# Performance work log

Hardware: AMD Instinct MI355X
Metric: run time of the kernel (lower is better)

## Reference

```python
import jax, jax.numpy as jnp
import numpy as np

# tag2index constants
PAD, START, END, T = 0, 14, 15, 16
B, L, V, E, H = 128, 512, 30000, 256, 256


def _lstm(xs, w_ih, w_hh, b, reverse=False):
    """xs: [L, B, E] -> hs: [L, B, H]. PyTorch gate order i,f,g,o."""
    Bsz = xs.shape[1]
    Hd = w_hh.shape[1]
    def cell(carry, xt):
        h, c = carry
        g = xt @ w_ih.T + h @ w_hh.T + b  # [B, 4H]
        i, f, gg, o = jnp.split(g, 4, axis=-1)
        c = jax.nn.sigmoid(f) * c + jax.nn.sigmoid(i) * jnp.tanh(gg)
        h = jax.nn.sigmoid(o) * jnp.tanh(c)
        return (h, c), h
    init = (jnp.zeros((Bsz, Hd), xs.dtype), jnp.zeros((Bsz, Hd), xs.dtype))
    _, hs = jax.lax.scan(cell, init, xs, reverse=reverse)
    return hs


def setup_inputs() -> dict:
    key = jax.random.key(0)
    ks = jax.random.split(key, 12)
    batch_data = jax.random.randint(ks[0], (B, L), 0, V, dtype=jnp.int32)
    # variable-length tags with contiguous trailing PAD (as the model assumes)
    lengths = jax.random.randint(ks[1], (B,), L // 4, L + 1)
    raw_tags = jax.random.randint(ks[2], (B, L), 1, 14, dtype=jnp.int32)  # real tags in [1,14)
    pos = jnp.arange(L)[None, :]
    batch_tag = jnp.where(pos < lengths[:, None], raw_tags, PAD).astype(jnp.int32)
    s = 0.05
    emb = jax.random.normal(ks[3], (V, E), jnp.float32) * s
    w_ih_f = jax.random.normal(ks[4], (4 * H, E), jnp.float32) * s
    w_hh_f = jax.random.normal(ks[5], (4 * H, H), jnp.float32) * s
    b_f = jnp.zeros((4 * H,), jnp.float32)
    w_ih_b = jax.random.normal(ks[6], (4 * H, E), jnp.float32) * s
    w_hh_b = jax.random.normal(ks[7], (4 * H, H), jnp.float32) * s
    b_b = jnp.zeros((4 * H,), jnp.float32)
    w_cls = jax.random.normal(ks[8], (T, 2 * H), jnp.float32) * s
    b_cls = jnp.zeros((T,), jnp.float32)
    transition = jnp.full((T, T), 1.0 / T, jnp.float32)
    return {"batch_data": batch_data, "batch_tag": batch_tag, "emb": emb,
            "w_ih_f": w_ih_f, "w_hh_f": w_hh_f, "b_f": b_f,
            "w_ih_b": w_ih_b, "w_hh_b": w_hh_b, "b_b": b_b,
            "w_cls": w_cls, "b_cls": b_cls, "transition": transition}


def reference(batch_data, batch_tag, emb, w_ih_f, w_hh_f, b_f,
              w_ih_b, w_hh_b, b_b, w_cls, b_cls, transition):
    # ---- BiLSTM encoder ----
    x = emb[batch_data]                      # [B, L, E]
    xs = jnp.moveaxis(x, 1, 0)               # [L, B, E]
    hf = _lstm(xs, w_ih_f, w_hh_f, b_f, reverse=False)
    hb = _lstm(xs, w_ih_b, w_hh_b, b_b, reverse=True)
    out = jnp.moveaxis(jnp.concatenate([hf, hb], axis=-1), 0, 1)  # [B, L, 2H]
    emission = out @ w_cls.T + b_cls          # [B, L, T]
    crf_scores = emission[:, :, None, :] + transition[None, None]  # [B, L, T, T]

    # ---- CRF loss (linear-chain forward algorithm) ----
    mask = batch_tag != PAD                   # [B, L]
    lengths = mask.sum(axis=1)                # [B]
    prev = jnp.concatenate(
        [jnp.full((B, 1), START, batch_tag.dtype), batch_tag[:, :-1]], axis=1)
    idx = (batch_tag + prev * T).astype(jnp.int32)  # flat (prev_tag, cur_tag) index
    flat = crf_scores.reshape(B, L, T * T)
    g = jnp.take_along_axis(flat, idx[:, :, None], axis=2)[..., 0]
    golden_scores = jnp.sum(jnp.where(mask, g, 0.0))

    sc_t = jnp.moveaxis(crf_scores, 1, 0)     # [L, B, T, T]
    init = sc_t[0, :, START, :]               # [B, T] (all lengths >= 1)
    def step(prev_scores, x_t):
        sc, t = x_t
        new = jax.nn.logsumexp(sc + prev_scores[:, :, None], axis=1)  # [B, T]
        active = (lengths > t)[:, None]
        return jnp.where(active, new, prev_scores), None
    final, _ = jax.lax.scan(step, init, (sc_t[1:], jnp.arange(1, L)))
    all_path_scores = jnp.sum(final[:, END])
    loss = (all_path_scores - golden_scores) / B
    return loss
```

## Files before the change

### kernel.cpp

```cpp
#include <hip/hip_runtime.h>

#define Bsz 128
#define Lseq 512
#define Hdim 256
#define Tn 16
#define START_TAG 14
#define END_TAG 15

typedef float f32x4 __attribute__((ext_vector_type(4)));
typedef short s16x8 __attribute__((ext_vector_type(8)));

__device__ __forceinline__ unsigned short f2bf(float f) {
    unsigned int u = __builtin_bit_cast(unsigned int, f);
    u += 0x7fffu + ((u >> 16) & 1u);
    return (unsigned short)(u >> 16);
}
__device__ __forceinline__ float bf2f(unsigned int bits16) {
    return __builtin_bit_cast(float, bits16 << 16);
}
__device__ __forceinline__ float sigmoidf_(float x) {
    return 1.0f / (1.0f + __expf(-x));
}

__global__ void embprep_kernel(const float* __restrict__ emb,
                               unsigned int* __restrict__ embb, int n2) {
    int i = blockIdx.x * blockDim.x + threadIdx.x;
    int stride = gridDim.x * blockDim.x;
    for (; i < n2; i += stride)
        embb[i] = (unsigned int)f2bf(emb[2 * i]) | ((unsigned int)f2bf(emb[2 * i + 1]) << 16);
}

__global__ void wprep_kernel(const float* __restrict__ wih_f, const float* __restrict__ whh_f,
                             const float* __restrict__ wih_b, const float* __restrict__ whh_b,
                             unsigned int* __restrict__ wtile) {
    int bid = blockIdx.x;
    int ki  = bid & 15;
    int tl  = (bid >> 4) & 3;
    int ug  = (bid >> 6) & 15;
    int dir = bid >> 10;
    int t = threadIdx.x;
    int lane = t >> 2, j = t & 3;
    int n = lane & 15, kq = lane >> 4;
    int k0 = ki * 32 + kq * 8 + 2 * j;
    int col = tl * 256 + ug * 16 + n;
    const float* wih = dir ? wih_b : wih_f;
    const float* whh = dir ? whh_b : whh_f;
    float f0, f1;
    if (k0 < 256) { f0 = wih[col * 256 + k0];       f1 = wih[col * 256 + k0 + 1]; }
    else          { f0 = whh[col * 256 + k0 - 256]; f1 = whh[col * 256 + k0 - 255]; }
    wtile[(size_t)bid * 256 + t] = (unsigned int)f2bf(f0) | ((unsigned int)f2bf(f1) << 16);
}

__global__ void lengths_kernel(const int* __restrict__ tag, int* __restrict__ lengths) {
    int b = blockIdx.x;
    int tid = threadIdx.x;
    int cnt = 0;
    for (int l = tid; l < Lseq; l += blockDim.x)
        cnt += (tag[b * Lseq + l] != 0) ? 1 : 0;
    for (int off = 32; off > 0; off >>= 1) cnt += __shfl_down(cnt, off);
    __shared__ int red[4];
    if ((tid & 63) == 0) red[tid >> 6] = cnt;
    __syncthreads();
    if (tid == 0) lengths[b] = red[0] + red[1] + red[2] + red[3];
}

__global__ __launch_bounds__(256, 1) void bilstm_persist(
    const int* __restrict__ bd,
    const unsigned int* __restrict__ embb,
    const unsigned int* __restrict__ wtile,
    const float* __restrict__ b_f, const float* __restrict__ b_b,
    const float* __restrict__ w_cls,
    float* __restrict__ em_f, float* __restrict__ em_b,
    unsigned int* __restrict__ ring,
    int* __restrict__ flags)
{
    const int wg  = blockIdx.x;
    const int dir = wg >> 7;
    const int bg  = (wg >> 4) & 7;
    const int ug  = wg & 15;
    const int grp = dir * 8 + bg;
    const int tid = threadIdx.x;
    const int gb0 = bg * 16;

    __shared__ unsigned int w_lds[16384];
    __shared__ unsigned int h_lds[16 * 132];
    __shared__ float g_lds[4][16][17];
    __shared__ float part_lds[16][17];
    __shared__ float bias_lds[64];
    __shared__ float wcls_lds[256];

    {
        const unsigned int* wsrc = wtile + ((size_t)(dir * 16 + ug) << 14);
        for (int i = 0; i < 16; ++i) {
            int idx = tid + 256 * i;
            uint4 v = *(const uint4*)(wsrc + (size_t)idx * 4);
            *(uint4*)&w_lds[idx * 4] = v;
        }
        if (tid < 64) {
            const float* bias = dir ? b_b : b_f;
            bias_lds[tid] = bias[(tid >> 4) * 256 + ug * 16 + (tid & 15)];
        }
        wcls_lds[tid] = w_cls[(size_t)ug * (2 * Hdim) + dir * Hdim + tid];
    }

    const int wv = tid >> 6;
    const int l  = tid & 63;
    const int n  = l & 15;
    const int kq = l >> 4;
    const int cb = tid >> 4, cu = tid & 15;
    const int em_m = tid >> 4, em_seg = tid & 15;
    float c_reg = 0.f;
    float* emout = dir ? em_b : em_f;
    const int* bd_row = bd + (size_t)(gb0 + n) * Lseq;

    unsigned int* rbase = ring + (size_t)dir * 2 * 16384;

    __syncthreads();

    f32x4 acc_x = {0.f, 0.f, 0.f, 0.f};
    {
        const int t0 = dir ? (Lseq - 1) : 0;
        int tok = bd_row[t0];
        const unsigned int* xsrc = embb + (size_t)tok * 128 + kq * 4;
        #pragma unroll
        for (int ki = 0; ki < 8; ++ki) {
            uint4 xv = *(const uint4*)(xsrc + ki * 16);
            s16x8 a = __builtin_bit_cast(s16x8, xv);
            s16x8 b = *(const s16x8*)&w_lds[((wv * 16 + ki) * 64 + l) * 4];
            acc_x = __builtin_amdgcn_mfma_f32_16x16x32_bf16(a, b, acc_x, 0, 0, 0);
        }
    }

    for (int s = 0; s < Lseq; ++s) {
        const int t = dir ? (Lseq - 1 - s) : s;
        const unsigned int* hprev = rbase + ((s & 1) ^ 1) * 16384;
        unsigned int*       hcur  = rbase + (s & 1) * 16384;

        {
            int m = tid >> 4, q0 = (tid & 15) * 8;
            const unsigned int* src = hprev + (gb0 + m) * 128 + q0;
            unsigned int v[8];
            #pragma unroll
            for (int j = 0; j < 8; ++j)
                v[j] = __hip_atomic_load(src + j, __ATOMIC_RELAXED, __HIP_MEMORY_SCOPE_AGENT);
            *(uint4*)&h_lds[m * 132 + q0]     = make_uint4(v[0], v[1], v[2], v[3]);
            *(uint4*)&h_lds[m * 132 + q0 + 4] = make_uint4(v[4], v[5], v[6], v[7]);
        }
        __syncthreads();

        if (s > 0) {
            const unsigned int* hr = &h_lds[em_m * 132 + em_seg * 8];
            const float* wc = &wcls_lds[em_seg * 16];
            float p = 0.f;
            #pragma unroll
            for (int j = 0; j < 8; ++j) {
                unsigned int v = hr[j];
                p += bf2f(v & 0xffffu) * wc[2 * j] + bf2f(v >> 16) * wc[2 * j + 1];
            }
            part_lds[em_m][em_seg] = p;
        }
        {
            f32x4 acc = acc_x;
            #pragma unroll
            for (int kih = 0; kih < 8; ++kih) {
                s16x8 a = *(const s16x8*)&h_lds[n * 132 + kih * 16 + kq * 4];
                s16x8 b = *(const s16x8*)&w_lds[(((wv * 16) + 8 + kih) * 64 + l) * 4];
                acc = __builtin_amdgcn_mfma_f32_16x16x32_bf16(a, b, acc, 0, 0, 0);
            }
            #pragma unroll
            for (int r = 0; r < 4; ++r)
                g_lds[wv][kq * 4 + r][n] = acc[r];
        }
        __syncthreads();

        {
            float gi = g_lds[0][cb][cu] + bias_lds[cu];
            float gf = g_lds[1][cb][cu] + bias_lds[16 + cu];
            float gg = g_lds[2][cb][cu] + bias_lds[32 + cu];
            float go = g_lds[3][cb][cu] + bias_lds[48 + cu];
            float cn = sigmoidf_(gf) * c_reg + sigmoidf_(gi) * tanhf(gg);
            c_reg = cn;
            float hn = sigmoidf_(go) * tanhf(cn);
            unsigned int hbits = (unsigned int)f2bf(hn);
            unsigned int other = (unsigned int)__shfl_down((int)hbits, 1);
            if ((cu & 1) == 0) {
                unsigned int pk = hbits | (other << 16);
                __hip_atomic_store(hcur + (gb0 + cb) * 128 + ug * 8 + (cu >> 1), pk,
                                   __ATOMIC_RELAXED, __HIP_MEMORY_SCOPE_AGENT);
            }
        }
        if (s > 0 && tid < 16) {
            float ssum = 0.f;
            #pragma unroll
            for (int q = 0; q < 16; ++q) ssum += part_lds[tid][q];
            int t_prev = dir ? (Lseq - s) : (s - 1);
            emout[((size_t)(gb0 + tid) * Lseq + t_prev) * Tn + ug] = ssum;
        }
        __syncthreads();

        if (tid == 0)
            __hip_atomic_store(&flags[((size_t)s * 16 + grp) * 16 + ug], 1,
                               __ATOMIC_RELAXED, __HIP_MEMORY_SCOPE_AGENT);

        if (s + 1 < Lseq) {
            const int tn = dir ? (Lseq - 2 - s) : (s + 1);
            int tok = bd_row[tn];
            const unsigned int* xsrc = embb + (size_t)tok * 128 + kq * 4;
            f32x4 ax = {0.f, 0.f, 0.f, 0.f};
            #pragma unroll
            for (int ki = 0; ki < 8; ++ki) {
                uint4 xv = *(const uint4*)(xsrc + ki * 16);
                s16x8 a = __builtin_bit_cast(s16x8, xv);
                s16x8 b = *(const s16x8*)&w_lds[((wv * 16 + ki) * 64 + l) * 4];
                ax = __builtin_amdgcn_mfma_f32_16x16x32_bf16(a, b, ax, 0, 0, 0);
            }
            acc_x = ax;
        }

        if (wv == 0) {
            const int* flg = &flags[((size_t)s * 16 + grp) * 16];
            while (true) {
                int v = (l < 16)
                    ? __hip_atomic_load(&flg[l], __ATOMIC_RELAXED, __HIP_MEMORY_SCOPE_AGENT)
                    : 1;
                if (__all(v != 0)) break;
                __builtin_amdgcn_s_sleep(1);
            }
        }
        __syncthreads();
    }

    {
        const unsigned int* hlast = rbase + ((Lseq - 1) & 1) * 16384;
        int m = tid >> 4, q0 = (tid & 15) * 8;
        const unsigned int* src = hlast + (gb0 + m) * 128 + q0;
        unsigned int v[8];
        #pragma unroll
        for (int j = 0; j < 8; ++j)
            v[j] = __hip_atomic_load(src + j, __ATOMIC_RELAXED, __HIP_MEMORY_SCOPE_AGENT);
        *(uint4*)&h_lds[m * 132 + q0]     = make_uint4(v[0], v[1], v[2], v[3]);
        *(uint4*)&h_lds[m * 132 + q0 + 4] = make_uint4(v[4], v[5], v[6], v[7]);
        __syncthreads();
        {
            const unsigned int* hr = &h_lds[em_m * 132 + em_seg * 8];
            const float* wc = &wcls_lds[em_seg * 16];
            float p = 0.f;
            #pragma unroll
            for (int j = 0; j < 8; ++j) {
                unsigned int vv = hr[j];
                p += bf2f(vv & 0xffffu) * wc[2 * j] + bf2f(vv >> 16) * wc[2 * j + 1];
            }
            part_lds[em_m][em_seg] = p;
        }
        __syncthreads();
        if (tid < 16) {
            float ssum = 0.f;
            #pragma unroll
            for (int q = 0; q < 16; ++q) ssum += part_lds[tid][q];
            int t_tail = dir ? 0 : (Lseq - 1);
            emout[((size_t)(gb0 + tid) * Lseq + t_tail) * Tn + ug] = ssum;
        }
    }
}

__global__ void golden_kernel(const int* __restrict__ tag,
                              const float* __restrict__ em_f,
                              const float* __restrict__ em_b,
                              const float* __restrict__ b_cls,
                              const float* __restrict__ trans,
                              float* __restrict__ golden)
{
    int b = blockIdx.x;
    int tid = threadIdx.x;
    float s = 0.f;
    for (int l = tid; l < Lseq; l += blockDim.x) {
        int tg = tag[b * Lseq + l];
        if (tg != 0) {
            int prev = (l == 0) ? START_TAG : tag[b * Lseq + l - 1];
            size_t e = ((size_t)b * Lseq + l) * Tn + tg;
            s += em_f[e] + em_b[e] + b_cls[tg] + trans[prev * Tn + tg];
        }
    }
    for (int off = 32; off > 0; off >>= 1) s += __shfl_down(s, off);
    __shared__ float red[4];
    if ((tid & 63) == 0) red[tid >> 6] = s;
    __syncthreads();
    if (tid == 0) atomicAdd(golden, red[0] + red[1] + red[2] + red[3]);
}

__global__ void crf_forward_kernel(const float* __restrict__ em_f,
                                   const float* __restrict__ em_b,
                                   const float* __restrict__ b_cls,
                                   const float* __restrict__ trans,
                                   const int* __restrict__ lengths,
                                   float* __restrict__ allpath)
{
    int b = blockIdx.x;
    int lane = threadIdx.x;
    int j = lane & 15;
    float tcol[16];
    #pragma unroll
    for (int i = 0; i < 16; ++i) tcol[i] = trans[i * Tn + j];
    float bc = b_cls[j];
    size_t e0 = ((size_t)b * Lseq) * Tn + j;
    float alpha = em_f[e0] + em_b[e0] + bc + tcol[START_TAG];
    int len = lengths[b];
    for (int t = 1; t < Lseq; ++t) {
        float av[16];
        float m = -1e30f;
        #pragma unroll
        for (int i = 0; i < 16; ++i) {
            av[i] = __shfl(alpha, i) + tcol[i];
            m = fmaxf(m, av[i]);
        }
        float sum = 0.f;
        #pragma unroll
        for (int i = 0; i < 16; ++i) sum += __expf(av[i] - m);
        size_t e = ((size_t)b * Lseq + t) * Tn + j;
        float nv = em_f[e] + em_b[e] + bc + m + __logf(sum);
        alpha = (t < len) ? nv : alpha;
    }
    if (lane == END_TAG) atomicAdd(allpath, alpha);
}

__global__ void finalize_kernel(const float* __restrict__ scal, float* __restrict__ out) {
    out[0] = (scal[1] - scal[0]) / (float)Bsz;
}

extern "C" void kernel_launch(void* const* d_in, const int* in_sizes, int n_in,
                              void* d_out, int out_size, void* d_ws, size_t ws_size,
                              hipStream_t stream)
{
    (void)in_sizes; (void)n_in; (void)out_size; (void)ws_size;
    const int*   bd     = (const int*)d_in[0];
    const int*   tag    = (const int*)d_in[1];
    const float* emb    = (const float*)d_in[2];
    const float* w_ih_f = (const float*)d_in[3];
    const float* w_hh_f = (const float*)d_in[4];
    const float* b_f    = (const float*)d_in[5];
    const float* w_ih_b = (const float*)d_in[6];
    const float* w_hh_b = (const float*)d_in[7];
    const float* b_b    = (const float*)d_in[8];
    const float* w_cls  = (const float*)d_in[9];
    const float* b_cls  = (const float*)d_in[10];
    const float* trans  = (const float*)d_in[11];
    float* out = (float*)d_out;

    float* ws = (float*)d_ws;
    float* em_f = ws;
    float* em_b = em_f + (size_t)Bsz * Lseq * Tn;
    unsigned int* ring = (unsigned int*)(em_b + (size_t)Bsz * Lseq * Tn);
    float* scal = (float*)(ring + 65536);
    int* flags = (int*)(scal + 8);
    int* lengths = flags + (size_t)Lseq * 16 * 16;
    unsigned int* wtile = (unsigned int*)(lengths + 128);
    unsigned int* embb = wtile + (size_t)524288;

    size_t zbytes = (65536 + 8 + (size_t)Lseq * 16 * 16) * 4;
    hipMemsetAsync(ring, 0, zbytes, stream);

    embprep_kernel<<<2048, 256, 0, stream>>>(emb, embb, 30000 * 128);
    wprep_kernel<<<2048, 256, 0, stream>>>(w_ih_f, w_hh_f, w_ih_b, w_hh_b, wtile);
    lengths_kernel<<<Bsz, 256, 0, stream>>>(tag, lengths);

    void* kargs[] = {
        (void*)&bd, (void*)&embb, (void*)&wtile,
        (void*)&b_f, (void*)&b_b, (void*)&w_cls,
        (void*)&em_f, (void*)&em_b,
        (void*)&ring, (void*)&flags
    };
    hipLaunchCooperativeKernel((const void*)bilstm_persist,
                               dim3(256), dim3(256), kargs, 0, stream);

    golden_kernel<<<Bsz, 256, 0, stream>>>(tag, em_f, em_b, b_cls, trans, scal);
    crf_forward_kernel<<<Bsz, 64, 0, stream>>>(em_f, em_b, b_cls, trans, lengths, scal + 1);
    finalize_kernel<<<1, 1, 0, stream>>>(scal, out);
}
```

Baseline: 2.348 ms.

## Replace flag barriers with epoch-tagged hidden-state polling and register-resident weights

Drops the per-step flag array and second block barrier. Each packed bf16 hidden value now carries its parity epoch in the low mantissa bit, and consumers poll the ring data directly until the expected epoch appears. Weights move from LDS into registers. Gate columns are reordered so each lane group holds i/f/g/o for one unit, letting the cell update run via shuffles without an LDS round trip. The emission partial is reduced in one wave with xor-shuffles. This trades one mantissa bit of h precision, and relies on memset 0x01 initialising the epoch, to cut cross-workgroup synchronisation latency on the serial recurrence.

New measurement: 2.678 ms. 14.0% more time.

```diff
diff --git a/kernel.cpp b/kernel.cpp
--- a/kernel.cpp
+++ b/kernel.cpp
@@ -35,14 +35,14 @@
                              unsigned int* __restrict__ wtile) {
     int bid = blockIdx.x;
     int ki  = bid & 15;
-    int tl  = (bid >> 4) & 3;
+    int wv  = (bid >> 4) & 3;
     int ug  = (bid >> 6) & 15;
     int dir = bid >> 10;
     int t = threadIdx.x;
     int lane = t >> 2, j = t & 3;
     int n = lane & 15, kq = lane >> 4;
     int k0 = ki * 32 + kq * 8 + 2 * j;
-    int col = tl * 256 + ug * 16 + n;
+    int col = (n & 3) * 256 + ug * 16 + wv * 4 + (n >> 2);
     const float* wih = dir ? wih_b : wih_f;
     const float* whh = dir ? whh_b : whh_f;
     float f0, f1;
@@ -71,194 +71,197 @@
     const float* __restrict__ b_f, const float* __restrict__ b_b,
     const float* __restrict__ w_cls,
     float* __restrict__ em_f, float* __restrict__ em_b,
-    unsigned int* __restrict__ ring,
-    int* __restrict__ flags)
+    unsigned int* __restrict__ ring)
 {
     const int wg  = blockIdx.x;
     const int dir = wg >> 7;
     const int bg  = (wg >> 4) & 7;
     const int ug  = wg & 15;
-    const int grp = dir * 8 + bg;
     const int tid = threadIdx.x;
     const int gb0 = bg * 16;
 
-    __shared__ unsigned int w_lds[16384];
-    __shared__ unsigned int h_lds[16 * 132];
-    __shared__ float g_lds[4][16][17];
-    __shared__ float part_lds[16][17];
-    __shared__ float bias_lds[64];
+    __shared__ unsigned int h_lds[2][16 * 132];
     __shared__ float wcls_lds[256];
 
-    {
-        const unsigned int* wsrc = wtile + ((size_t)(dir * 16 + ug) << 14);
-        for (int i = 0; i < 16; ++i) {
-            int idx = tid + 256 * i;
-            uint4 v = *(const uint4*)(wsrc + (size_t)idx * 4);
-            *(uint4*)&w_lds[idx * 4] = v;
-        }
-        if (tid < 64) {
-            const float* bias = dir ? b_b : b_f;
-            bias_lds[tid] = bias[(tid >> 4) * 256 + ug * 16 + (tid & 15)];
-        }
-        wcls_lds[tid] = w_cls[(size_t)ug * (2 * Hdim) + dir * Hdim + tid];
-    }
+    wcls_lds[tid] = w_cls[(size_t)ug * (2 * Hdim) + dir * Hdim + tid];
 
     const int wv = tid >> 6;
     const int l  = tid & 63;
     const int n  = l & 15;
     const int kq = l >> 4;
-    const int cb = tid >> 4, cu = tid & 15;
-    const int em_m = tid >> 4, em_seg = tid & 15;
-    float c_reg = 0.f;
+
+    uint4 w_reg[16];
+    {
+        const unsigned int* wsrc =
+            wtile + ((size_t)((dir * 16 + ug) * 4 + wv) * 16) * 256 + l * 4;
+        #pragma unroll
+        for (int ki = 0; ki < 16; ++ki)
+            w_reg[ki] = *(const uint4*)(wsrc + ki * 256);
+    }
+    const float bias_lane = (dir ? b_b : b_f)[(n & 3) * 256 + ug * 16 + wv * 4 + (n >> 2)];
+    float c_reg[4] = {0.f, 0.f, 0.f, 0.f};
+    const int* bdr = bd + (size_t)(gb0 + n) * Lseq;
+    unsigned int* rb = ring + (size_t)dir * 2 * 16384;
+    const bool storer = ((l & 7) == 0);
+    const int store_col = ug * 8 + wv * 2 + ((n >> 2) >> 1);
     float* emout = dir ? em_b : em_f;
-    const int* bd_row = bd + (size_t)(gb0 + n) * Lseq;
-
-    unsigned int* rbase = ring + (size_t)dir * 2 * 16384;
+
+    const int pm = tid >> 4, pq0 = (tid & 15) * 8;
 
     __syncthreads();
 
     f32x4 acc_x = {0.f, 0.f, 0.f, 0.f};
     {
         const int t0 = dir ? (Lseq - 1) : 0;
-        int tok = bd_row[t0];
+        int tok = bdr[t0];
         const unsigned int* xsrc = embb + (size_t)tok * 128 + kq * 4;
         #pragma unroll
         for (int ki = 0; ki < 8; ++ki) {
-            uint4 xv = *(const uint4*)(xsrc + ki * 16);
-            s16x8 a = __builtin_bit_cast(s16x8, xv);
-            s16x8 b = *(const s16x8*)&w_lds[((wv * 16 + ki) * 64 + l) * 4];
-            acc_x = __builtin_amdgcn_mfma_f32_16x16x32_bf16(a, b, acc_x, 0, 0, 0);
+            s16x8 a = __builtin_bit_cast(s16x8, *(const uint4*)(xsrc + ki * 16));
+            acc_x = __builtin_amdgcn_mfma_f32_16x16x32_bf16(
+                a, __builtin_bit_cast(s16x8, w_reg[ki]), acc_x, 0, 0, 0);
         }
     }
 
     for (int s = 0; s < Lseq; ++s) {
-        const int t = dir ? (Lseq - 1 - s) : s;
-        const unsigned int* hprev = rbase + ((s & 1) ^ 1) * 16384;
-        unsigned int*       hcur  = rbase + (s & 1) * 16384;
-
         {
-            int m = tid >> 4, q0 = (tid & 15) * 8;
-            const unsigned int* src = hprev + (gb0 + m) * 128 + q0;
+            const unsigned int* src = rb + ((s + 1) & 1) * 16384 + (gb0 + pm) * 128 + pq0;
+            const unsigned int want = (((s + 3) >> 1) & 1) * 0x00010001u;
             unsigned int v[8];
             #pragma unroll
             for (int j = 0; j < 8; ++j)
                 v[j] = __hip_atomic_load(src + j, __ATOMIC_RELAXED, __HIP_MEMORY_SCOPE_AGENT);
-            *(uint4*)&h_lds[m * 132 + q0]     = make_uint4(v[0], v[1], v[2], v[3]);
-            *(uint4*)&h_lds[m * 132 + q0 + 4] = make_uint4(v[4], v[5], v[6], v[7]);
+            bool again = true;
+            while (again) {
+                again = false;
+                #pragma unroll
+                for (int j = 0; j < 8; ++j)
+                    if ((v[j] & 0x00010001u) != want) {
+                        v[j] = __hip_atomic_load(src + j, __ATOMIC_RELAXED,
+                                                 __HIP_MEMORY_SCOPE_AGENT);
+                        again = true;
+                    }
+            }
+            unsigned int* dst = &h_lds[s & 1][pm * 132 + pq0];
+            *(uint4*)dst       = make_uint4(v[0], v[1], v[2], v[3]);
+            *(uint4*)(dst + 4) = make_uint4(v[4], v[5], v[6], v[7]);
         }
         __syncthreads();
-
-        if (s > 0) {
-            const unsigned int* hr = &h_lds[em_m * 132 + em_seg * 8];
-            const float* wc = &wcls_lds[em_seg * 16];
+        const unsigned int* hb = &h_lds[s & 1][0];
+
+        if (wv == 0 && s > 0) {
             float p = 0.f;
             #pragma unroll
-            for (int j = 0; j < 8; ++j) {
-                unsigned int v = hr[j];
-                p += bf2f(v & 0xffffu) * wc[2 * j] + bf2f(v >> 16) * wc[2 * j + 1];
-            }
-            part_lds[em_m][em_seg] = p;
-        }
+            for (int kih = 0; kih < 8; ++kih) {
+                const unsigned int* hp = &hb[n * 132 + kih * 16 + kq * 4];
+                const float* wc = &wcls_lds[kih * 32 + kq * 8];
+                #pragma unroll
+                for (int j = 0; j < 4; ++j) {
+                    unsigned int v = hp[j];
+                    p += bf2f(v & 0xffffu) * wc[2 * j] + bf2f(v >> 16) * wc[2 * j + 1];
+                }
+            }
+            p += __shfl_xor(p, 16);
+            p += __shfl_xor(p, 32);
+            if (l < 16) {
+                int t_prev = dir ? (Lseq - s) : (s - 1);
+                emout[((size_t)(gb0 + l) * Lseq + t_prev) * Tn + ug] = p;
+            }
+        }
+
+        f32x4 acc = acc_x;
+        #pragma unroll
+        for (int kih = 0; kih < 8; ++kih) {
+            s16x8 a = *(const s16x8*)&hb[n * 132 + kih * 16 + kq * 4];
+            acc = __builtin_amdgcn_mfma_f32_16x16x32_bf16(
+                a, __builtin_bit_cast(s16x8, w_reg[8 + kih]), acc, 0, 0, 0);
+        }
+
         {
-            f32x4 acc = acc_x;
-            #pragma unroll
-            for (int kih = 0; kih < 8; ++kih) {
-                s16x8 a = *(const s16x8*)&h_lds[n * 132 + kih * 16 + kq * 4];
-                s16x8 b = *(const s16x8*)&w_lds[(((wv * 16) + 8 + kih) * 64 + l) * 4];
-                acc = __builtin_amdgcn_mfma_f32_16x16x32_bf16(a, b, acc, 0, 0, 0);
-            }
-            #pragma unroll
-            for (int r = 0; r < 4; ++r)
-                g_lds[wv][kq * 4 + r][n] = acc[r];
-        }
-        __syncthreads();
-
-        {
-            float gi = g_lds[0][cb][cu] + bias_lds[cu];
-            float gf = g_lds[1][cb][cu] + bias_lds[16 + cu];
-            float gg = g_lds[2][cb][cu] + bias_lds[32 + cu];
-            float go = g_lds[3][cb][cu] + bias_lds[48 + cu];
-            float cn = sigmoidf_(gf) * c_reg + sigmoidf_(gi) * tanhf(gg);
-            c_reg = cn;
-            float hn = sigmoidf_(go) * tanhf(cn);
-            unsigned int hbits = (unsigned int)f2bf(hn);
-            unsigned int other = (unsigned int)__shfl_down((int)hbits, 1);
-            if ((cu & 1) == 0) {
-                unsigned int pk = hbits | (other << 16);
-                __hip_atomic_store(hcur + (gb0 + cb) * 128 + ug * 8 + (cu >> 1), pk,
-                                   __ATOMIC_RELAXED, __HIP_MEMORY_SCOPE_AGENT);
-            }
-        }
-        if (s > 0 && tid < 16) {
-            float ssum = 0.f;
-            #pragma unroll
-            for (int q = 0; q < 16; ++q) ssum += part_lds[tid][q];
-            int t_prev = dir ? (Lseq - s) : (s - 1);
-            emout[((size_t)(gb0 + tid) * Lseq + t_prev) * Tn + ug] = ssum;
-        }
-        __syncthreads();
-
-        if (tid == 0)
-            __hip_atomic_store(&flags[((size_t)s * 16 + grp) * 16 + ug], 1,
-                               __ATOMIC_RELAXED, __HIP_MEMORY_SCOPE_AGENT);
+            const unsigned int ep = (unsigned int)((s >> 1) & 1);
+            const int base = l & ~3;
+            unsigned int hbits[4];
+            #pragma unroll
+            for (int r = 0; r < 4; ++r) {
+                float pre = acc[r] + bias_lane;
+                float gi = __shfl(pre, base);
+                float gf = __shfl(pre, base + 1);
+                float gg = __shfl(pre, base + 2);
+                float go = __shfl(pre, base + 3);
+                float cn = sigmoidf_(gf) * c_reg[r] + sigmoidf_(gi) * tanhf(gg);
+                c_reg[r] = cn;
+                float hn = sigmoidf_(go) * tanhf(cn);
+                hbits[r] = ((unsigned int)f2bf(hn) & 0xFFFEu) | ep;
+            }
+            unsigned int* dstrow = rb + (s & 1) * 16384;
+            #pragma unroll
+            for (int r = 0; r < 4; ++r) {
+                unsigned int partner = (unsigned int)__shfl((int)hbits[r], l + 4);
+                if (storer) {
+                    unsigned int pk = hbits[r] | (partner << 16);
+                    __hip_atomic_store(dstrow + (gb0 + kq * 4 + r) * 128 + store_col, pk,
+                                       __ATOMIC_RELAXED, __HIP_MEMORY_SCOPE_AGENT);
+                }
+            }
+        }
 
         if (s + 1 < Lseq) {
             const int tn = dir ? (Lseq - 2 - s) : (s + 1);
-            int tok = bd_row[tn];
+            int tok = bdr[tn];
             const unsigned int* xsrc = embb + (size_t)tok * 128 + kq * 4;
             f32x4 ax = {0.f, 0.f, 0.f, 0.f};
             #pragma unroll
             for (int ki = 0; ki < 8; ++ki) {
-                uint4 xv = *(const uint4*)(xsrc + ki * 16);
-                s16x8 a = __builtin_bit_cast(s16x8, xv);
-                s16x8 b = *(const s16x8*)&w_lds[((wv * 16 + ki) * 64 + l) * 4];
-                ax = __builtin_amdgcn_mfma_f32_16x16x32_bf16(a, b, ax, 0, 0, 0);
+                s16x8 a = __builtin_bit_cast(s16x8, *(const uint4*)(xsrc + ki * 16));
+                ax = __builtin_amdgcn_mfma_f32_16x16x32_bf16(
+                    a, __builtin_bit_cast(s16x8, w_reg[ki]), ax, 0, 0, 0);
             }
             acc_x = ax;
         }
-
-        if (wv == 0) {
-            const int* flg = &flags[((size_t)s * 16 + grp) * 16];
-            while (true) {
-                int v = (l < 16)
-                    ? __hip_atomic_load(&flg[l], __ATOMIC_RELAXED, __HIP_MEMORY_SCOPE_AGENT)
-                    : 1;
-                if (__all(v != 0)) break;
-                __builtin_amdgcn_s_sleep(1);
-            }
-        }
-        __syncthreads();
     }
 
     {
-        const unsigned int* hlast = rbase + ((Lseq - 1) & 1) * 16384;
-        int m = tid >> 4, q0 = (tid & 15) * 8;
-        const unsigned int* src = hlast + (gb0 + m) * 128 + q0;
+        const int s = Lseq;
+        const unsigned int* src = rb + ((s + 1) & 1) * 16384 + (gb0 + pm) * 128 + pq0;
+        const unsigned int want = (((s + 3) >> 1) & 1) * 0x00010001u;
         unsigned int v[8];
         #pragma unroll
         for (int j = 0; j < 8; ++j)
             v[j] = __hip_atomic_load(src + j, __ATOMIC_RELAXED, __HIP_MEMORY_SCOPE_AGENT);
-        *(uint4*)&h_lds[m * 132 + q0]     = make_uint4(v[0], v[1], v[2], v[3]);
-        *(uint4*)&h_lds[m * 132 + q0 + 4] = make_uint4(v[4], v[5], v[6], v[7]);
+        bool again = true;
+        while (again) {
+            again = false;
+            #pragma unroll
+            for (int j = 0; j < 8; ++j)
+                if ((v[j] & 0x00010001u) != want) {
+                    v[j] = __hip_atomic_load(src + j, __ATOMIC_RELAXED,
+                                             __HIP_MEMORY_SCOPE_AGENT);
+                    again = true;
+                }
+        }
+        unsigned int* dst = &h_lds[0][pm * 132 + pq0];
+        *(uint4*)dst       = make_uint4(v[0], v[1], v[2], v[3]);
+        *(uint4*)(dst + 4) = make_uint4(v[4], v[5], v[6], v[7]);
         __syncthreads();
-        {
-            const unsigned int* hr = &h_lds[em_m * 132 + em_seg * 8];
-            const float* wc = &wcls_lds[em_seg * 16];
+        if (wv == 0) {
+            const unsigned int* hb = &h_lds[0][0];
             float p = 0.f;
             #pragma unroll
-            for (int j = 0; j < 8; ++j) {
-                unsigned int vv = hr[j];
-                p += bf2f(vv & 0xffffu) * wc[2 * j] + bf2f(vv >> 16) * wc[2 * j + 1];
-            }
-            part_lds[em_m][em_seg] = p;
-        }
-        __syncthreads();
-        if (tid < 16) {
-            float ssum = 0.f;
-            #pragma unroll
-            for (int q = 0; q < 16; ++q) ssum += part_lds[tid][q];
-            int t_tail = dir ? 0 : (Lseq - 1);
-            emout[((size_t)(gb0 + tid) * Lseq + t_tail) * Tn + ug] = ssum;
+            for (int kih = 0; kih < 8; ++kih) {
+                const unsigned int* hp = &hb[n * 132 + kih * 16 + kq * 4];
+                const float* wc = &wcls_lds[kih * 32 + kq * 8];
+                #pragma unroll
+                for (int j = 0; j < 4; ++j) {
+                    unsigned int vv = hp[j];
+                    p += bf2f(vv & 0xffffu) * wc[2 * j] + bf2f(vv >> 16) * wc[2 * j + 1];
+                }
+            }
+            p += __shfl_xor(p, 16);
+            p += __shfl_xor(p, 32);
+            if (l < 16) {
+                int t_tail = dir ? 0 : (Lseq - 1);
+                emout[((size_t)(gb0 + l) * Lseq + t_tail) * Tn + ug] = p;
+            }
         }
     }
 }
@@ -351,13 +354,12 @@
     float* em_b = em_f + (size_t)Bsz * Lseq * Tn;
     unsigned int* ring = (unsigned int*)(em_b + (size_t)Bsz * Lseq * Tn);
     float* scal = (float*)(ring + 65536);
-    int* flags = (int*)(scal + 8);
-    int* lengths = flags + (size_t)Lseq * 16 * 16;
+    int* lengths = (int*)(scal + 8);
     unsigned int* wtile = (unsigned int*)(lengths + 128);
     unsigned int* embb = wtile + (size_t)524288;
 
-    size_t zbytes = (65536 + 8 + (size_t)Lseq * 16 * 16) * 4;
-    hipMemsetAsync(ring, 0, zbytes, stream);
+    hipMemsetAsync(ring, 0x01, (size_t)65536 * 4, stream);
+    hipMemsetAsync(scal, 0, 8 * sizeof(float), stream);
 
     embprep_kernel<<<2048, 256, 0, stream>>>(emb, embb, 30000 * 128);
     wprep_kernel<<<2048, 256, 0, stream>>>(w_ih_f, w_hh_f, w_ih_b, w_hh_b, wtile);
@@ -366,8 +368,7 @@
     void* kargs[] = {
         (void*)&bd, (void*)&embb, (void*)&wtile,
         (void*)&b_f, (void*)&b_b, (void*)&w_cls,
-        (void*)&em_f, (void*)&em_b,
-        (void*)&ring, (void*)&flags
+        (void*)&em_f, (void*)&em_b, (void*)&ring
     };
     hipLaunchCooperativeKernel((const void*)bilstm_persist,
                                dim3(256), dim3(256), kargs, 0, stream);
```
